# Optimization experiments

Measured on AMD Instinct MI355X. Metric: run time of the kernel, lower is better.

The kernel has to match this reference:

```python
import jax, jax.numpy as jnp
import numpy as np

B, N0 = 16384, 2048
NUM_CLASSES, NUM_CLUSTERS, NDIM = 12, 24, 4
W_SCALE = 0.02  # keep logits in a sane range for softmax


def setup_inputs() -> dict:
    key = jax.random.key(0)
    ks = jax.random.split(key, 7)
    return {
        "x": jax.random.normal(ks[0], (B, N0), dtype=jnp.float32),
        "W_fc": jax.random.normal(ks[1], (N0, NUM_CLASSES), dtype=jnp.float32) * W_SCALE,
        "b_fc": jax.random.normal(ks[2], (NUM_CLASSES,), dtype=jnp.float32) * W_SCALE,
        "W_bin": jax.random.normal(ks[3], (NUM_CLASSES, N0, NUM_CLUSTERS), dtype=jnp.float32) * W_SCALE,
        "b_bin": jax.random.normal(ks[4], (NUM_CLASSES, NUM_CLUSTERS), dtype=jnp.float32) * W_SCALE,
        "W_res": jax.random.normal(ks[5], (NUM_CLASSES, N0, NDIM), dtype=jnp.float32) * W_SCALE,
        "b_res": jax.random.normal(ks[6], (NUM_CLASSES, NDIM), dtype=jnp.float32) * W_SCALE,
    }


def reference(x, W_fc, b_fc, W_bin, b_bin, W_res, b_res):
    # x: [B, N0] pre-extracted features (feature_model output)
    bsz = x.shape[0]
    C = W_bin.shape[0]

    # category head
    y0 = x @ W_fc + b_fc                                   # [B, C]
    Pc = jax.nn.softmax(y0, axis=1)                        # [B, C]

    # grouped per-class bin linears as one batched GEMM -> [B, K, C]
    y1 = jnp.einsum('bd,cdk->bkc', x, W_bin) + b_bin.T[None]
    Pl = jax.nn.softmax(y1, axis=1)                        # softmax over clusters
    Plc = Pl * Pc[:, None, :]                              # [B, K, C]

    # joint argmax over (cluster, class); torch flatten of [B,K,C] -> ic = ind % C
    ind = jnp.argmax(Plc.reshape(bsz, -1), axis=1)
    ic = ind % C                                           # selected class per row

    # direct gather replaces one-hot scatter + bmm
    y1_sel = jnp.take_along_axis(y1, ic[:, None, None], axis=2)[..., 0]   # [B, K]

    # grouped per-class residual linears -> [B, ndim, C], then gather
    y2 = jnp.einsum('bd,cdn->bnc', x, W_res) + b_res.T[None]
    y2_sel = jnp.take_along_axis(y2, ic[:, None, None], axis=2)[..., 0]   # [B, ndim]

    return (y0, y1_sel, y2_sel, Plc)
```

## Files before the change

kernel.cpp:

```cpp
#include <hip/hip_runtime.h>
#include <math.h>

#define BROWS 16384
#define N0    2048
#define NCLS  12
#define NCLU  24
#define NDIM  4
#define NCOL  348
#define NPAD  384
#define NTILE 24

#define OUT0_OFF 0
#define OUT1_OFF (BROWS * NCLS)
#define OUT2_OFF (OUT1_OFF + BROWS * NCLU)
#define OUT3_OFF (OUT2_OFF + BROWS * NDIM)

typedef __attribute__((ext_vector_type(8))) short bf16x8;
typedef __attribute__((ext_vector_type(4))) float f32x4;
typedef unsigned short ushort_t;

__device__ __forceinline__ unsigned short f2bf(float f) {
    unsigned u = __float_as_uint(f);
    u += 0x7fffu + ((u >> 16) & 1u);
    return (unsigned short)(u >> 16);
}
__device__ __forceinline__ float bf2f(unsigned short h) {
    return __uint_as_float(((unsigned)h) << 16);
}
__device__ __forceinline__ void cvt8(float4 a, float4 b, bf16x8& h, bf16x8& l) {
    float f[8] = {a.x, a.y, a.z, a.w, b.x, b.y, b.z, b.w};
    #pragma unroll
    for (int i = 0; i < 8; ++i) {
        unsigned short hi = f2bf(f[i]);
        h[i] = (short)hi;
        l[i] = (short)f2bf(f[i] - bf2f(hi));
    }
}

__device__ __forceinline__ void load_lds16(const void* g, void* l) {
    __builtin_amdgcn_global_load_lds((const __attribute__((address_space(1))) void*)g,
                                     (__attribute__((address_space(3))) void*)l, 16, 0, 0);
}

__device__ __forceinline__ float fused_w(const float* __restrict__ W_fc,
                                         const float* __restrict__ W_bin,
                                         const float* __restrict__ W_res,
                                         int col, int d) {
    float w = 0.0f;
    if (col < NCLS) {
        w = W_fc[d * NCLS + col];
    } else if (col < 12 + NCLU * NCLS) {
        int jj = col - 12;
        int k = jj / NCLS, c = jj - k * NCLS;
        w = W_bin[((size_t)c * N0 + d) * NCLU + k];
    } else if (col < NCOL) {
        int jj = col - 300;
        int n = jj / NCLS, c = jj - n * NCLS;
        w = W_res[((size_t)c * N0 + d) * NDIM + n];
    }
    return w;
}

__global__ void jcp_repack3(const float* __restrict__ W_fc, const float* __restrict__ b_fc,
                            const float* __restrict__ W_bin, const float* __restrict__ b_bin,
                            const float* __restrict__ W_res, const float* __restrict__ b_res,
                            ushort_t* __restrict__ Bph, ushort_t* __restrict__ Bpl,
                            float* __restrict__ bias) {
    int t = blockIdx.x * 256 + threadIdx.x;
    if (t >= NTILE * 64 * 64) return;
    const int lane = t & 63;
    const int kb   = (t >> 6) & 63;
    const int J    = t >> 12;
    const int col  = J * 16 + (lane & 15);
    const int k0   = kb * 32 + (lane >> 4) * 8;

    bf16x8 h, l;
    #pragma unroll
    for (int i = 0; i < 8; ++i) {
        float w = fused_w(W_fc, W_bin, W_res, col, k0 + i);
        unsigned short hi = f2bf(w);
        h[i] = (short)hi;
        l[i] = (short)f2bf(w - bf2f(hi));
    }
    *(bf16x8*)(Bph + (size_t)t * 8) = h;
    *(bf16x8*)(Bpl + (size_t)t * 8) = l;

    if (t < NPAD) {
        int jb = t;
        float bv = 0.0f;
        if (jb < NCLS) {
            bv = b_fc[jb];
        } else if (jb < 12 + NCLU * NCLS) {
            int jj = jb - 12;
            int k = jj / NCLS, c = jj - k * NCLS;
            bv = b_bin[c * NCLU + k];
        } else if (jb < NCOL) {
            int jj = jb - 300;
            int n = jj / NCLS, c = jj - n * NCLS;
            bv = b_res[c * NDIM + n];
        }
        bias[jb] = bv;
    }
}

__global__ __launch_bounds__(256, 4) void jcp_gemm4(const float* __restrict__ x,
                                                    const ushort_t* __restrict__ Bph,
                                                    const ushort_t* __restrict__ Bpl,
                                                    const float* __restrict__ bias,
                                                    float* __restrict__ Y) {
    __shared__ float Lx[2 * 2048];

    const int tid  = threadIdx.x;
    const int wid  = tid >> 6;
    const int lane = tid & 63;
    const int quad = lane >> 4;
    const int l16  = lane & 15;
    const int wrow = (wid & 1) * 32;
    const int wct  = (wid >> 1) * 3;
    const int rbase = blockIdx.y * 64;
    const int jbase = blockIdx.x * 96;

    const int dr = lane >> 3;
    const int dc = (lane & 7) ^ dr;
    const float* gsrc0 = x + (size_t)(rbase + 8 * (2 * wid) + dr) * N0 + dc * 4;
    const float* gsrc1 = x + (size_t)(rbase + 8 * (2 * wid + 1) + dr) * N0 + dc * 4;
    const int ldst0 = (2 * wid) * 256;
    const int ldst1 = (2 * wid + 1) * 256;

    const int s = l16 & 7;
    const int pos1 = (2 * quad) ^ s;
    const int o1 = pos1 * 4;
    const int o2 = (pos1 ^ 1) * 4;
    const int ro0 = (wrow + l16) * 32;
    const int ro1 = (wrow + 16 + l16) * 32;

    const ushort_t* pBh = Bph + (size_t)lane * 8;
    const ushort_t* pBl = Bpl + (size_t)lane * 8;
    int Jt[3];
    #pragma unroll
    for (int j = 0; j < 3; ++j) Jt[j] = (jbase / 16 + wct + j) * 32768;

    f32x4 acc[2][3];
    #pragma unroll
    for (int i = 0; i < 2; ++i)
        #pragma unroll
        for (int j = 0; j < 3; ++j)
            acc[i][j] = f32x4{0.f, 0.f, 0.f, 0.f};

    load_lds16(gsrc0, &Lx[ldst0]);
    load_lds16(gsrc1, &Lx[ldst1]);
    __syncthreads();

    int p = 0;
    for (int it = 0; it < 64; ++it) {
        bf16x8 bh[3], bl[3];
        #pragma unroll
        for (int j = 0; j < 3; ++j) {
            bh[j] = *(const bf16x8*)(pBh + Jt[j] + it * 512);
            bl[j] = *(const bf16x8*)(pBl + Jt[j] + it * 512);
        }
        if (it < 63) {
            load_lds16(gsrc0 + (it + 1) * 32, &Lx[(p ^ 1) * 2048 + ldst0]);
            load_lds16(gsrc1 + (it + 1) * 32, &Lx[(p ^ 1) * 2048 + ldst1]);
        }
        const int pb = p * 2048;
        float4 f0a = *(const float4*)&Lx[pb + ro0 + o1];
        float4 f0b = *(const float4*)&Lx[pb + ro0 + o2];
        float4 f1a = *(const float4*)&Lx[pb + ro1 + o1];
        float4 f1b = *(const float4*)&Lx[pb + ro1 + o2];
        bf16x8 Ah[2], Al[2];
        cvt8(f0a, f0b, Ah[0], Al[0]);
        cvt8(f1a, f1b, Ah[1], Al[1]);

        #pragma unroll
        for (int j = 0; j < 3; ++j)
            #pragma unroll
            for (int i = 0; i < 2; ++i) {
                acc[i][j] = __builtin_amdgcn_mfma_f32_16x16x32_bf16(Ah[i], bh[j], acc[i][j], 0, 0, 0);
                acc[i][j] = __builtin_amdgcn_mfma_f32_16x16x32_bf16(Al[i], bh[j], acc[i][j], 0, 0, 0);
                acc[i][j] = __builtin_amdgcn_mfma_f32_16x16x32_bf16(Ah[i], bl[j], acc[i][j], 0, 0, 0);
            }
        __syncthreads();
        p ^= 1;
    }

    #pragma unroll
    for (int j = 0; j < 3; ++j) {
        const int col = jbase + wct * 16 + 16 * j + l16;
        const float bj = bias[col];
        #pragma unroll
        for (int i = 0; i < 2; ++i) {
            float* yp = Y + (size_t)(rbase + wrow + i * 16 + quad * 4) * NPAD + col;
            yp[0 * NPAD] = acc[i][j][0] + bj;
            yp[1 * NPAD] = acc[i][j][1] + bj;
            yp[2 * NPAD] = acc[i][j][2] + bj;
            yp[3 * NPAD] = acc[i][j][3] + bj;
        }
    }
}

#define LROW 388

__global__ __launch_bounds__(256) void jcp_head3(const float* __restrict__ Y,
                                                 float* __restrict__ out) {
    __shared__ float Ly[16 * LROW];
    const int tid = threadIdx.x;
    const int r0  = blockIdx.x * 16;

    #pragma unroll
    for (int jj = 0; jj < 6; ++jj) {
        int f = tid + jj * 256;
        int row = f / 96, c4 = f - row * 96;
        float4 v = *(const float4*)(Y + (size_t)(r0 + row) * NPAD + c4 * 4);
        *(float4*)&Ly[row * LROW + c4 * 4] = v;
    }
    __syncthreads();

    const int grp = tid >> 4;
    const int c   = tid & 15;
    const bool on = (c < NCLS);
    const int r   = r0 + grp;
    const float* y = &Ly[grp * LROW];

    float y0c = on ? y[c] : -INFINITY;
    float m0 = y0c;
    #pragma unroll
    for (int m = 8; m >= 1; m >>= 1) m0 = fmaxf(m0, __shfl_xor(m0, m, 16));
    float e0 = on ? expf(y0c - m0) : 0.0f;
    float s0 = e0;
    #pragma unroll
    for (int m = 8; m >= 1; m >>= 1) s0 += __shfl_xor(s0, m, 16);
    const float Pc = e0 / s0;

    float v[NCLU];
    float mc = -INFINITY;
    #pragma unroll
    for (int k = 0; k < NCLU; ++k) {
        v[k] = y[12 + k * NCLS + c];
        mc = fmaxf(mc, v[k]);
    }
    float sc = 0.0f;
    #pragma unroll
    for (int k = 0; k < NCLU; ++k) sc += expf(v[k] - mc);
    const float rs = Pc / sc;

    float y2c[NDIM];
    #pragma unroll
    for (int n = 0; n < NDIM; ++n) y2c[n] = y[300 + n * NCLS + c];

    float best = -INFINITY;
    int bk = 0;
    float* lrow = &Ly[grp * LROW];
    #pragma unroll
    for (int k = 0; k < NCLU; ++k) {
        const float p = expf(v[k] - mc) * rs;
        if (on) lrow[k * NCLS + c] = p;
        if (p > best) { best = p; bk = k; }
    }
    int flat = bk * NCLS + c;
    if (!on) { best = -INFINITY; flat = 1 << 30; }

    #pragma unroll
    for (int m = 8; m >= 1; m >>= 1) {
        const float op = __shfl_xor(best, m, 16);
        const int   of = __shfl_xor(flat, m, 16);
        if (op > best || (op == best && of < flat)) { best = op; flat = of; }
    }
    const int ic = flat % NCLS;

    if (on) out[OUT0_OFF + (size_t)r * NCLS + c] = y0c;
    if (c == ic) {
        float* o1 = out + OUT1_OFF + (size_t)r * NCLU;
        #pragma unroll
        for (int k = 0; k < NCLU; ++k) o1[k] = v[k];
        float* o2 = out + OUT2_OFF + (size_t)r * NDIM;
        #pragma unroll
        for (int n = 0; n < NDIM; ++n) o2[n] = y2c[n];
    }

    __syncthreads();
    #pragma unroll
    for (int jj = 0; jj < 5; ++jj) {
        int f = tid + jj * 256;
        if (f < 1152) {
            int row = f / 72, c4 = f - row * 72;
            *(float4*)(out + OUT3_OFF + (size_t)(r0 + row) * (NCLU * NCLS) + c4 * 4) =
                *(float4*)&Ly[row * LROW + c4 * 4];
        }
    }
}

extern "C" void kernel_launch(void* const* d_in, const int* in_sizes, int n_in,
                              void* d_out, int out_size, void* d_ws, size_t ws_size,
                              hipStream_t stream) {
    const float* x     = (const float*)d_in[0];
    const float* W_fc  = (const float*)d_in[1];
    const float* b_fc  = (const float*)d_in[2];
    const float* W_bin = (const float*)d_in[3];
    const float* b_bin = (const float*)d_in[4];
    const float* W_res = (const float*)d_in[5];
    const float* b_res = (const float*)d_in[6];
    float* out = (float*)d_out;

    ushort_t* Bph  = (ushort_t*)d_ws;
    ushort_t* Bpl  = Bph + NTILE * 64 * 64 * 8;
    float*    bias = (float*)(Bpl + NTILE * 64 * 64 * 8);
    float*    Yb   = bias + NPAD;

    jcp_repack3<<<384, 256, 0, stream>>>(W_fc, b_fc, W_bin, b_bin, W_res, b_res,
                                         Bph, Bpl, bias);
    dim3 grid(NPAD / 96, BROWS / 64);
    jcp_gemm4<<<grid, 256, 0, stream>>>(x, Bph, Bpl, bias, Yb);
    jcp_head3<<<BROWS / 16, 256, 0, stream>>>(Yb, out);
}
```

Before: 319.5 us.

## Pre-split x into bf16 hi/lo in swizzled layout before a new GEMM kernel

Adds a separate pass that converts fp32 x into packed bf16 high/low halves in a swizzled tile layout. A new GEMM kernel streams these tiles into LDS with direct async loads, uses smaller 48-column tiles with higher occupancy, and remaps block indices so that blocks on the same XCD share rows. This takes the per-tile fp32-to-bf16 conversion out of the GEMM inner loop and halves the bytes the GEMM reads from LDS. In exchange it adds a full extra write and re-read of x through workspace (about 134 MB), and x is now read 8 times across column tiles instead of 4. It falls back to the old kernel if the workspace is too small.

```diff
diff --git a/kernel.cpp b/kernel.cpp
--- a/kernel.cpp
+++ b/kernel.cpp
@@ -103,6 +103,110 @@
     }
 }
 
+__global__ __launch_bounds__(256) void jcp_xcvt(const float* __restrict__ x,
+                                                ushort_t* __restrict__ Xc) {
+    const int t0 = blockIdx.x * 256 + threadIdx.x;
+    #pragma unroll
+    for (int i = 0; i < 4; ++i) {
+        const size_t t = (size_t)t0 + (size_t)i * 1048576;
+        const float4 a = *(const float4*)(x + t * 8);
+        const float4 b = *(const float4*)(x + t * 8 + 4);
+        bf16x8 h, l;
+        cvt8(a, b, h, l);
+        const size_t r  = t >> 8;
+        const int    oc = (int)(t & 255);
+        const int    kb = oc >> 2, o = oc & 3;
+        ushort_t* dst = Xc + (r * 64 + kb) * 64;
+        *(bf16x8*)(dst + o * 8)      = h;
+        *(bf16x8*)(dst + 32 + o * 8) = l;
+    }
+}
+
+__global__ __launch_bounds__(256, 8) void jcp_gemm5(const ushort_t* __restrict__ Xc,
+                                                    const ushort_t* __restrict__ Bph,
+                                                    const ushort_t* __restrict__ Bpl,
+                                                    const float* __restrict__ bias,
+                                                    float* __restrict__ Y) {
+    __shared__ ushort_t Lx[2 * 4096];
+
+    const int tid  = threadIdx.x;
+    const int wid  = tid >> 6;
+    const int lane = tid & 63;
+    const int quad = lane >> 4;
+    const int l16  = lane & 15;
+
+    const int g   = blockIdx.x;
+    const int xcd = g & 7;
+    const int jj  = g >> 3;
+    const int by  = xcd * 32 + (jj >> 3);
+    const int bx  = jj & 7;
+    const int rbase = by * 64;
+    const int jbase = bx * 48;
+    const int wrow  = wid * 16;
+
+    const int r0 = tid >> 3;
+    const int c0 = tid & 7;
+    const int o0 = c0 ^ (r0 & 7);
+    const ushort_t* gsrc0 = Xc + (size_t)(rbase + r0) * 4096 + o0 * 8;
+    const ushort_t* gsrc1 = gsrc0 + (size_t)32 * 4096;
+    const int ldst0 = tid * 8;
+    const int ldst1 = ldst0 + 2048;
+
+    const int R     = wrow + l16;
+    const int haddr = R * 64 + ((quad ^ (R & 7)) << 3);
+
+    const ushort_t* pBh = Bph + (size_t)lane * 8;
+    const ushort_t* pBl = Bpl + (size_t)lane * 8;
+    int Jt[3];
+    #pragma unroll
+    for (int j = 0; j < 3; ++j) Jt[j] = (bx * 3 + j) * 32768;
+
+    f32x4 acc[3];
+    #pragma unroll
+    for (int j = 0; j < 3; ++j) acc[j] = f32x4{0.f, 0.f, 0.f, 0.f};
+
+    load_lds16(gsrc0, &Lx[ldst0]);
+    load_lds16(gsrc1, &Lx[ldst1]);
+    __syncthreads();
+
+    int p = 0;
+    for (int it = 0; it < 64; ++it) {
+        if (it < 63) {
+            load_lds16(gsrc0 + (it + 1) * 64, &Lx[(p ^ 1) * 4096 + ldst0]);
+            load_lds16(gsrc1 + (it + 1) * 64, &Lx[(p ^ 1) * 4096 + ldst1]);
+        }
+        bf16x8 bh[3], bl[3];
+        #pragma unroll
+        for (int j = 0; j < 3; ++j) {
+            bh[j] = *(const bf16x8*)(pBh + Jt[j] + it * 512);
+            bl[j] = *(const bf16x8*)(pBl + Jt[j] + it * 512);
+        }
+        const ushort_t* lb = &Lx[p * 4096];
+        bf16x8 Ah = *(const bf16x8*)(lb + haddr);
+        bf16x8 Al = *(const bf16x8*)(lb + (haddr ^ 32));
+
+        #pragma unroll
+        for (int j = 0; j < 3; ++j) {
+            acc[j] = __builtin_amdgcn_mfma_f32_16x16x32_bf16(Ah, bh[j], acc[j], 0, 0, 0);
+            acc[j] = __builtin_amdgcn_mfma_f32_16x16x32_bf16(Al, bh[j], acc[j], 0, 0, 0);
+            acc[j] = __builtin_amdgcn_mfma_f32_16x16x32_bf16(Ah, bl[j], acc[j], 0, 0, 0);
+        }
+        __syncthreads();
+        p ^= 1;
+    }
+
+    #pragma unroll
+    for (int j = 0; j < 3; ++j) {
+        const int col = jbase + 16 * j + l16;
+        const float bj = bias[col];
+        float* yp = Y + (size_t)(rbase + wrow + quad * 4) * NPAD + col;
+        yp[0 * NPAD] = acc[j][0] + bj;
+        yp[1 * NPAD] = acc[j][1] + bj;
+        yp[2 * NPAD] = acc[j][2] + bj;
+        yp[3 * NPAD] = acc[j][3] + bj;
+    }
+}
+
 __global__ __launch_bounds__(256, 4) void jcp_gemm4(const float* __restrict__ x,
                                                     const ushort_t* __restrict__ Bph,
                                                     const ushort_t* __restrict__ Bpl,
@@ -306,10 +410,21 @@
     ushort_t* Bpl  = Bph + NTILE * 64 * 64 * 8;
     float*    bias = (float*)(Bpl + NTILE * 64 * 64 * 8);
     float*    Yb   = bias + NPAD;
+    ushort_t* Xc   = (ushort_t*)(Yb + (size_t)BROWS * NPAD);
+
+    const size_t need = (size_t)(NTILE * 64 * 64 * 8) * 2 * sizeof(ushort_t)
+                      + NPAD * sizeof(float)
+                      + (size_t)BROWS * NPAD * sizeof(float)
+                      + (size_t)BROWS * 4096 * sizeof(ushort_t);
 
     jcp_repack3<<<384, 256, 0, stream>>>(W_fc, b_fc, W_bin, b_bin, W_res, b_res,
                                          Bph, Bpl, bias);
-    dim3 grid(NPAD / 96, BROWS / 64);
-    jcp_gemm4<<<grid, 256, 0, stream>>>(x, Bph, Bpl, bias, Yb);
+    if (ws_size >= need) {
+        jcp_xcvt<<<4096, 256, 0, stream>>>(x, Xc);
+        jcp_gemm5<<<2048, 256, 0, stream>>>(Xc, Bph, Bpl, bias, Yb);
+    } else {
+        dim3 grid(NPAD / 96, BROWS / 64);
+        jcp_gemm4<<<grid, 256, 0, stream>>>(x, Bph, Bpl, bias, Yb);
+    }
     jcp_head3<<<BROWS / 16, 256, 0, stream>>>(Yb, out);
 }
```

Result: slower. 402.8 us (+26.1%).
